# Kernel tuning notes

Hardware: AMD Instinct MI355X
Metric: run time of the kernel (lower is better)

Reference implementation:

```python
import jax, jax.numpy as jnp
import numpy as np

DENSE_SIZE = 2048
BATCH = 64
MAX_SPIKES = 1024


def setup_inputs() -> dict:
    key = jax.random.key(0)
    k_w, k_ids, k_ns = jax.random.split(key, 3)
    # weights ~ N(0, 2) as in tf.random_normal_initializer(0., 2., 42)
    W = jax.random.normal(k_w, (DENSE_SIZE, DENSE_SIZE), dtype=jnp.float32) * 2.0
    spike_ids = jax.random.randint(k_ids, (BATCH, MAX_SPIKES), 0, DENSE_SIZE, dtype=jnp.int32)
    num_spikes = jax.random.randint(k_ns, (BATCH,), 0, MAX_SPIKES, dtype=jnp.int32)
    return {"spike_ids": spike_ids, "num_spikes": num_spikes, "W": W}


def reference(spike_ids, num_spikes, W):
    # Dense-weight x binary-sparse-vector matmul:
    # out[b, j] = sum_{i < num_spikes[b]} W[j, spike_ids[b, i]]
    # i.e. gather active columns of W and sum them.
    mask = (jnp.arange(MAX_SPIKES)[None, :] < num_spikes[:, None]).astype(W.dtype)  # [B, S]
    cols = jnp.take(W.T, spike_ids, axis=0)  # [B, S, D] gathered columns (rows of W.T)
    out = jnp.einsum('bs,bsd->bd', mask, cols)  # [B, D]
    return out
```

## Files before the change

kernel.cpp:

```cpp
#include <hip/hip_runtime.h>

#define DENSE 2048
#define BATCH 64
#define MAXS  1024

typedef __attribute__((ext_vector_type(8))) __bf16 bf16x8;
typedef __attribute__((ext_vector_type(4))) float f32x4;


__global__ __launch_bounds__(256) void hist_kernel(const int* __restrict__ ids,
                                                   const int* __restrict__ ns,
                                                   __bf16* __restrict__ Cbf) {
    __shared__ int cnt[DENSE];
    const int b = blockIdx.x;
    const int tid = threadIdx.x;
    ((int4*)cnt)[tid]       = int4{0, 0, 0, 0};
    ((int4*)cnt)[tid + 256] = int4{0, 0, 0, 0};
    __syncthreads();
    const int n = ns[b];
    const int4 v = ((const int4*)(ids + b * MAXS))[tid];
    const int base = tid * 4;
    if (base + 0 < n) atomicAdd(&cnt[v.x], 1);
    if (base + 1 < n) atomicAdd(&cnt[v.y], 1);
    if (base + 2 < n) atomicAdd(&cnt[v.z], 1);
    if (base + 3 < n) atomicAdd(&cnt[v.w], 1);
    __syncthreads();
    const int mt = b >> 4;
    const int bl = b & 15;
    const int l2 = bl | ((tid & 3) << 4);
    const size_t off = ((size_t)((tid >> 2) * 4 + mt) * 64 + l2) * 8;
    const int4 c0 = ((const int4*)cnt)[tid * 2];
    const int4 c1 = ((const int4*)cnt)[tid * 2 + 1];
    bf16x8 o;
    o[0] = (__bf16)(float)c0.x;  o[1] = (__bf16)(float)c0.y;
    o[2] = (__bf16)(float)c0.z;  o[3] = (__bf16)(float)c0.w;
    o[4] = (__bf16)(float)c1.x;  o[5] = (__bf16)(float)c1.y;
    o[6] = (__bf16)(float)c1.z;  o[7] = (__bf16)(float)c1.w;
    *(bf16x8*)(Cbf + off) = o;
}

__global__ __launch_bounds__(1024, 1) void spmm_kernel(const float* __restrict__ W,
                                                       const __bf16* __restrict__ Cbf,
                                                       float* __restrict__ out) {
    __shared__ float P[16][16][64];

    const int tid  = threadIdx.x;
    const int lane = tid & 63;
    const int wv   = tid >> 6;
    const int j0   = blockIdx.x * 16;
    const int ln   = lane & 15;
    const int lq   = lane >> 4;
    const int step0 = wv * 4;
    const float* wrow = W + (size_t)(j0 + ln) * DENSE;

    f32x4 w0[4], w1[4];
    #pragma unroll
    for (int s = 0; s < 4; ++s) {
        const int kbase = (step0 + s) * 32 + lq * 8;
        w0[s] = *(const f32x4*)(wrow + kbase);
        w1[s] = *(const f32x4*)(wrow + kbase + 4);
    }
    bf16x8 afr[4][4];
    #pragma unroll
    for (int s = 0; s < 4; ++s) {
        #pragma unroll
        for (int mt = 0; mt < 4; ++mt) {
            afr[s][mt] = *(const bf16x8*)(Cbf + ((size_t)((step0 + s) * 4 + mt) * 64 + lane) * 8);
        }
    }

    f32x4 acc[4];
    #pragma unroll
    for (int mt = 0; mt < 4; ++mt) acc[mt] = (f32x4)0.0f;
    #pragma unroll
    for (int s = 0; s < 4; ++s) {
        bf16x8 wb;
        #pragma unroll
        for (int i = 0; i < 4; ++i) {
            wb[i]     = (__bf16)w0[s][i];
            wb[i + 4] = (__bf16)w1[s][i];
        }
        #pragma unroll
        for (int mt = 0; mt < 4; ++mt) {
            acc[mt] = __builtin_amdgcn_mfma_f32_16x16x32_bf16(afr[s][mt], wb, acc[mt], 0, 0, 0);
        }
    }

    #pragma unroll
    for (int mt = 0; mt < 4; ++mt) {
        #pragma unroll
        for (int r = 0; r < 4; ++r) {
            P[wv][mt * 4 + r][lane] = acc[mt][r];
        }
    }
    __syncthreads();

    const int jloc  = tid & 15;
    const int brow  = tid >> 4;
    const int mt    = brow >> 4;
    const int bpart = brow & 15;
    const int lsrc  = ((bpart >> 2) << 4) | jloc;
    const int r     = bpart & 3;
    float v = 0.0f;
    #pragma unroll
    for (int w = 0; w < 16; ++w) v += P[w][mt * 4 + r][lsrc];
    out[(size_t)brow * DENSE + j0 + jloc] = v;
}

extern "C" void kernel_launch(void* const* d_in, const int* in_sizes, int n_in,
                              void* d_out, int out_size, void* d_ws, size_t ws_size,
                              hipStream_t stream) {
    const int*   ids = (const int*)d_in[0];
    const int*   ns  = (const int*)d_in[1];
    const float* W   = (const float*)d_in[2];
    float*  out = (float*)d_out;
    __bf16* Cbf = (__bf16*)d_ws;

    hipLaunchKernelGGL(hist_kernel, dim3(BATCH), dim3(256), 0, stream, ids, ns, Cbf);
    hipLaunchKernelGGL(spmm_kernel, dim3(DENSE / 16), dim3(1024), 0, stream, W, Cbf, out);
}
```

Baseline: 73.83 us.

## Fuse histogram and SpMM into one kernel with per-block packed LDS histograms

```diff
diff --git a/kernel.cpp b/kernel.cpp
--- a/kernel.cpp
+++ b/kernel.cpp
@@ -8,103 +8,97 @@
 typedef __attribute__((ext_vector_type(4))) float f32x4;
 
 
-__global__ __launch_bounds__(256) void hist_kernel(const int* __restrict__ ids,
-                                                   const int* __restrict__ ns,
-                                                   __bf16* __restrict__ Cbf) {
-    __shared__ int cnt[DENSE];
-    const int b = blockIdx.x;
-    const int tid = threadIdx.x;
-    ((int4*)cnt)[tid]       = int4{0, 0, 0, 0};
-    ((int4*)cnt)[tid + 256] = int4{0, 0, 0, 0};
-    __syncthreads();
-    const int n = ns[b];
-    const int4 v = ((const int4*)(ids + b * MAXS))[tid];
-    const int base = tid * 4;
-    if (base + 0 < n) atomicAdd(&cnt[v.x], 1);
-    if (base + 1 < n) atomicAdd(&cnt[v.y], 1);
-    if (base + 2 < n) atomicAdd(&cnt[v.z], 1);
-    if (base + 3 < n) atomicAdd(&cnt[v.w], 1);
-    __syncthreads();
-    const int mt = b >> 4;
-    const int bl = b & 15;
-    const int l2 = bl | ((tid & 3) << 4);
-    const size_t off = ((size_t)((tid >> 2) * 4 + mt) * 64 + l2) * 8;
-    const int4 c0 = ((const int4*)cnt)[tid * 2];
-    const int4 c1 = ((const int4*)cnt)[tid * 2 + 1];
-    bf16x8 o;
-    o[0] = (__bf16)(float)c0.x;  o[1] = (__bf16)(float)c0.y;
-    o[2] = (__bf16)(float)c0.z;  o[3] = (__bf16)(float)c0.w;
-    o[4] = (__bf16)(float)c1.x;  o[5] = (__bf16)(float)c1.y;
-    o[6] = (__bf16)(float)c1.z;  o[7] = (__bf16)(float)c1.w;
-    *(bf16x8*)(Cbf + off) = o;
-}
-
-__global__ __launch_bounds__(1024, 1) void spmm_kernel(const float* __restrict__ W,
-                                                       const __bf16* __restrict__ Cbf,
-                                                       float* __restrict__ out) {
-    __shared__ float P[16][16][64];
+__global__ __launch_bounds__(256, 2) void fused_kernel(
+        const int* __restrict__ ids, const int* __restrict__ ns,
+        const float* __restrict__ W, float* __restrict__ out) {
+    __shared__ unsigned int lds[16 * 1024];
 
     const int tid  = threadIdx.x;
+    const int bid  = blockIdx.x;
+    const int jt   = bid & 127;
+    const int bq   = bid >> 7;
     const int lane = tid & 63;
     const int wv   = tid >> 6;
-    const int j0   = blockIdx.x * 16;
     const int ln   = lane & 15;
     const int lq   = lane >> 4;
-    const int step0 = wv * 4;
+    const int j0   = jt * 16;
+    const int step0 = wv * 16;
     const float* wrow = W + (size_t)(j0 + ln) * DENSE;
 
-    f32x4 w0[4], w1[4];
     #pragma unroll
-    for (int s = 0; s < 4; ++s) {
+    for (int z = 0; z < 16; ++z)
+        ((int4*)lds)[z * 256 + tid] = int4{0, 0, 0, 0};
+
+    int4 idv[16];
+    const int* idbase = ids + (size_t)bq * 16 * MAXS;
+    #pragma unroll
+    for (int c = 0; c < 16; ++c)
+        idv[c] = ((const int4*)(idbase + c * MAXS))[tid];
+
+    f32x4 w0[16], w1[16];
+    #pragma unroll
+    for (int s = 0; s < 16; ++s) {
         const int kbase = (step0 + s) * 32 + lq * 8;
         w0[s] = *(const f32x4*)(wrow + kbase);
         w1[s] = *(const f32x4*)(wrow + kbase + 4);
     }
-    bf16x8 afr[4][4];
+
+    __syncthreads();
+
+    const int base = tid * 4;
     #pragma unroll
-    for (int s = 0; s < 4; ++s) {
+    for (int c = 0; c < 16; ++c) {
+        const int n = ns[bq * 16 + c];
+        const int4 v = idv[c];
+        const int ks[4] = {v.x, v.y, v.z, v.w};
         #pragma unroll
-        for (int mt = 0; mt < 4; ++mt) {
-            afr[s][mt] = *(const bf16x8*)(Cbf + ((size_t)((step0 + s) * 4 + mt) * 64 + lane) * 8);
+        for (int e = 0; e < 4; ++e) {
+            if (base + e < n) {
+                const unsigned k = (unsigned)ks[e];
+                const unsigned byte0 = ((unsigned)c << 12) | ((k >> 1) << 2);
+                const unsigned swz = byte0 ^ ((unsigned)(c & 7) << 4);
+                atomicAdd(&lds[swz >> 2], 1u << ((k & 1) << 4));
+            }
         }
     }
+    __syncthreads();
 
-    f32x4 acc[4];
+    f32x4 acc = (f32x4)0.0f;
     #pragma unroll
-    for (int mt = 0; mt < 4; ++mt) acc[mt] = (f32x4)0.0f;
-    #pragma unroll
-    for (int s = 0; s < 4; ++s) {
+    for (int s = 0; s < 16; ++s) {
+        const unsigned abyte = ((unsigned)ln << 12) + (unsigned)((step0 + s) * 64)
+                             + ((unsigned)lq << 4);
+        const uint4 cw = *(const uint4*)((const char*)lds + (abyte ^ ((unsigned)(ln & 7) << 4)));
+        bf16x8 a;
+        a[0] = (__bf16)(float)(cw.x & 0xFFFFu);  a[1] = (__bf16)(float)(cw.x >> 16);
+        a[2] = (__bf16)(float)(cw.y & 0xFFFFu);  a[3] = (__bf16)(float)(cw.y >> 16);
+        a[4] = (__bf16)(float)(cw.z & 0xFFFFu);  a[5] = (__bf16)(float)(cw.z >> 16);
+        a[6] = (__bf16)(float)(cw.w & 0xFFFFu);  a[7] = (__bf16)(float)(cw.w >> 16);
         bf16x8 wb;
         #pragma unroll
         for (int i = 0; i < 4; ++i) {
             wb[i]     = (__bf16)w0[s][i];
             wb[i + 4] = (__bf16)w1[s][i];
         }
-        #pragma unroll
-        for (int mt = 0; mt < 4; ++mt) {
-            acc[mt] = __builtin_amdgcn_mfma_f32_16x16x32_bf16(afr[s][mt], wb, acc[mt], 0, 0, 0);
-        }
+        acc = __builtin_amdgcn_mfma_f32_16x16x32_bf16(a, wb, acc, 0, 0, 0);
     }
 
+    __syncthreads();
+    float* P = (float*)lds;
     #pragma unroll
-    for (int mt = 0; mt < 4; ++mt) {
-        #pragma unroll
-        for (int r = 0; r < 4; ++r) {
-            P[wv][mt * 4 + r][lane] = acc[mt][r];
-        }
-    }
+    for (int r = 0; r < 4; ++r)
+        P[(wv * 4 + r) * 65 + lane] = acc[r];
     __syncthreads();
 
     const int jloc  = tid & 15;
-    const int brow  = tid >> 4;
-    const int mt    = brow >> 4;
-    const int bpart = brow & 15;
+    const int bpart = tid >> 4;
     const int lsrc  = ((bpart >> 2) << 4) | jloc;
     const int r     = bpart & 3;
     float v = 0.0f;
     #pragma unroll
-    for (int w = 0; w < 16; ++w) v += P[w][mt * 4 + r][lsrc];
-    out[(size_t)brow * DENSE + j0 + jloc] = v;
+    for (int w = 0; w < 4; ++w)
+        v += P[(w * 4 + r) * 65 + lsrc];
+    out[(size_t)(bq * 16 + bpart) * DENSE + j0 + jloc] = v;
 }
 
 extern "C" void kernel_launch(void* const* d_in, const int* in_sizes, int n_in,
@@ -114,8 +108,7 @@
     const int*   ns  = (const int*)d_in[1];
     const float* W   = (const float*)d_in[2];
     float*  out = (float*)d_out;
-    __bf16* Cbf = (__bf16*)d_ws;
+    (void)d_ws; (void)ws_size;
 
-    hipLaunchKernelGGL(hist_kernel, dim3(BATCH), dim3(256), 0, stream, ids, ns, Cbf);
-    hipLaunchKernelGGL(spmm_kernel, dim3(DENSE / 16), dim3(1024), 0, stream, W, Cbf, out);
+    hipLaunchKernelGGL(fused_kernel, dim3(512), dim3(256), 0, stream, ids, ns, W, out);
 }
```

New measurement: 76.79 us. +4.0%, slower.
